# Optimization experiments

Measured on AMD Instinct MI355X. Metric: run time of the kernel, lower is better.

The kernel has to match this reference:

```python
import jax, jax.numpy as jnp
import numpy as np

PI = 3.141592657  # constant used verbatim in the original module


def _shift(a, dy, dx):
    # out[i, j] = a[i + dy, j + dx], zero-padded at the border (matches conv2d padding=1)
    h, w = a.shape
    p = jnp.pad(a, 1)
    return jax.lax.dynamic_slice(p, (1 + dy, 1 + dx), (h, w))


def setup_inputs() -> dict:
    key = jax.random.key(0)
    h, w = 2048, 4096
    # realistic metric depth in [1, 80] meters
    depth = jax.random.uniform(key, (h, w), dtype=jnp.float32, minval=1.0, maxval=80.0)
    fx = fy = 1000.0
    cx, cy = w / 2.0, h / 2.0
    cam_param = jnp.array([[fx, 0.0, cx], [0.0, fy, cy], [0.0, 0.0, 1.0]], dtype=jnp.float32)
    return {"depth": depth, "cam_param": cam_param, "sign_filter": 1}


def _nim_forward(depth, cam_param, sign_filter):
    h, w = depth.shape
    fx = cam_param[0, 0]
    fy = cam_param[1, 1]
    cx = cam_param[0, 2]
    cy = cam_param[1, 2]

    v = jnp.arange(h, dtype=jnp.float32)[:, None]
    u = jnp.arange(w, dtype=jnp.float32)[None, :]

    Z = depth
    Y = Z * (v - cy) / fx  # original uses camParam[0,0] for Y as well
    X = Z * (u - cx) / fx
    neg = Y <= 0
    Z = jnp.where(neg, 0.0, Z)
    Y = jnp.where(neg, 0.0, Y)
    Z = jnp.where(jnp.isnan(Z), 0.0, Z)

    D = 1.0 / Z  # disparity-like map; inf where Z == 0, as in torch

    # Gx = [[0,0,0],[-1,0,1],[0,0,0]], Gy = [[0,-1,0],[0,0,0],[0,1,0]] (cross-correlation)
    Gu = _shift(D, 0, 1) - _shift(D, 0, -1)
    Gv = _shift(D, 1, 0) - _shift(D, -1, 0)
    nx_t = Gu * fx
    ny_t = Gv * fy

    phi = jnp.arctan(ny_t / nx_t) + PI
    a = jnp.cos(phi)
    b = jnp.sin(phi)

    # the 4 diff kernels compute X[i,j] - X[i+dy, j+dx] for these neighbor offsets
    dirs = ((-1, 0), (0, -1), (0, 1), (1, 0))

    def diffs(A):
        return jnp.stack([A - _shift(A, dy, dx) for dy, dx in dirs])  # (4, h, w)

    X_d, Y_d, Z_d = diffs(X), diffs(Y), diffs(Z)

    nz_i = -(nx_t[None] * X_d + ny_t[None] * Y_d) / Z_d  # (4, h, w)
    norm = jnp.sqrt(nx_t[None] ** 2 + ny_t[None] ** 2 + nz_i ** 2)
    nxv = nx_t[None] / norm
    nyv = ny_t[None] / norm
    nzv = nz_i / norm
    nxv = jnp.where(jnp.isnan(nxv), 0.0, nxv)
    nyv = jnp.where(jnp.isnan(nyv), 0.0, nyv)
    nzv = jnp.where(jnp.isnan(nzv), 0.0, nzv)

    if sign_filter:
        n_pos = jnp.sum(nzv > 0, axis=0, keepdims=True)
        n_neg = jnp.sum(nzv < 0, axis=0, keepdims=True)
        pos_mask = (n_pos >= n_neg) & (nzv > 0)
        neg_mask = (n_pos < n_neg) & (nzv < 0)
        fm = (pos_mask | neg_mask).astype(jnp.float32)
        nxv = nxv * fm
        nyv = nyv * fm
        nzv = nzv * fm

    theta = jnp.arctan((jnp.sum(nxv, 0) * a + jnp.sum(nyv, 0) * b) / jnp.sum(nzv, 0))
    nx = jnp.sin(theta) * a
    ny = jnp.sin(theta) * b
    nz = jnp.cos(theta)
    bad = jnp.isnan(nz)
    nx = jnp.where(bad, 0.0, nx)
    ny = jnp.where(bad, 0.0, ny)
    nz = jnp.where(bad, -1.0, nz)

    sign_map = jnp.where(ny > 0, -1.0, 1.0)
    return jnp.stack([nx * sign_map, ny * sign_map, nz * sign_map])  # (3, h, w)


def reference(depth, cam_param, sign_filter):
    return _nim_forward(depth, cam_param, sign_filter)
```

## Files before the change

### kernel.cpp

```cpp
#include <hip/hip_runtime.h>
#include <math.h>

#define HH 2048
#define WW 4096

__device__ __forceinline__ float rcp_f(float x){ return __builtin_amdgcn_rcpf(x); }
__device__ __forceinline__ float rsq_f(float x){ return __builtin_amdgcn_rsqf(x); }

typedef float vf2 __attribute__((ext_vector_type(2)));

__device__ __forceinline__ void st_nt2(float* p, float a, float b){
    vf2 v = {a, b};
    __builtin_nontemporal_store(v, (vf2*)p);
}

__global__ __launch_bounds__(256, 6)
void nim_kernel(const float* __restrict__ depth,
                const float* __restrict__ cam,
                const int*   __restrict__ signf,
                float* __restrict__ out)
{
    const int j0 = (blockIdx.x * 256 + threadIdx.x) * 2;
    const int i  = blockIdx.y;
    const size_t HW  = (size_t)HH * WW;
    const size_t idx = (size_t)i * WW + j0;

    const float cy = cam[5];

    if ((float)i <= cy + 1.0f){
        st_nt2(out + idx,         0.f, 0.f);
        st_nt2(out + HW + idx,    0.f, 0.f);
        st_nt2(out + 2*HW + idx, -1.f,-1.f);
        return;
    }

    const float fx = cam[0], cx = cam[2], fy = cam[4];
    const float inv_fx = rcp_f(fx);
    const int   sf = signf[0];

    const float rf_u = ((float)(i - 1) - cy) * inv_fx;
    const float rf_c = ((float)i       - cy) * inv_fx;
    const float rf_d = ((float)(i + 1) - cy) * inv_fx;

    const float* rowc = depth + (size_t)i * WW + j0;
    const float* rowu = depth + (size_t)(i - 1) * WW + j0;

    float dc[4], du[2], dd[2];
    {
        const vf2 a = *(const vf2*)rowc;
        dc[1] = a.x; dc[2] = a.y;
        const vf2 ua = *(const vf2*)rowu;
        du[0] = ua.x; du[1] = ua.y;
    }
    const bool lv = (j0 > 0);
    const bool rv = (j0 + 2 < WW);
    dc[0] = lv ? rowc[-1] : 0.f;
    dc[3] = rv ? rowc[2]  : 0.f;

    const bool dv = (i + 1 < HH);
    if (dv){
        const vf2 da = *(const vf2*)(depth + (size_t)(i + 1) * WW + j0);
        dd[0] = da.x; dd[1] = da.y;
    } else {
        dd[0] = 0.f; dd[1] = 0.f;
    }

    float Dc[4], Du[2], Dd[2];
#pragma unroll
    for (int t = 0; t < 4; ++t) Dc[t] = rcp_f(dc[t]);
    if (!lv) Dc[0] = 0.f;
    if (!rv) Dc[3] = 0.f;
#pragma unroll
    for (int t = 0; t < 2; ++t){
        Du[t] = rcp_f(du[t]);
        Dd[t] = dv ? rcp_f(dd[t]) : 0.f;
    }

    const float jb = ((float)(j0 - 1) - cx) * inv_fx;

    float ox[2], oy[2], oz[2];
#pragma unroll
    for (int p = 0; p < 2; ++p){
        const float cfl = jb + (float)p       * inv_fx;
        const float cfc = jb + (float)(p + 1) * inv_fx;
        const float cfr = jb + (float)(p + 2) * inv_fx;
        const float CZ  = dc[p + 1];

        const float nx = (Dc[p + 2] - Dc[p]) * fx;
        const float ny = (Dd[p] - Du[p]) * fy;
        const float r2 = nx * nx + ny * ny;
        const float rr = rsq_f(r2);
        const float rs = copysignf(rr, nx);
        const float a  = -nx * rs;
        const float b  = -ny * rs;

        float hk[4], vzk[4];
        int npos = 0, nneg = 0;
#pragma unroll
        for (int k = 0; k < 4; ++k){
            float NZ, Xd, Yd;
            if (k == 0){ NZ = du[p];     const float w0 = CZ - NZ;
                         Xd = cfc * w0;  Yd = rf_c * CZ - rf_u * NZ; }
            else if (k == 1){ NZ = dc[p];     Xd = cfc * CZ - cfl * NZ;
                              Yd = rf_c * (CZ - NZ); }
            else if (k == 2){ NZ = dc[p + 2]; Xd = cfc * CZ - cfr * NZ;
                              Yd = rf_c * (CZ - NZ); }
            else            { NZ = dd[p];     const float w0 = CZ - NZ;
                              Xd = cfc * w0;  Yd = rf_c * CZ - rf_d * NZ; }
            const float w   = CZ - NZ;
            const float g   = nx * Xd + ny * Yd;
            const float arg = (r2 * w) * w + g * g;
            const float rn  = rsq_f(arg);
            float h  = fabsf(w) * rn;
            float vz = -g * copysignf(rn, w);
            const bool za = (arg == 0.f);
            if (za) h = 0.f;
            if (za || (w == 0.f)) vz = 0.f;
            hk[k] = h; vzk[k] = vz;
            npos += (vz > 0.f);
            nneg += (vz < 0.f);
        }

        const bool posm = (npos >= nneg);
        float H = 0.f, sz = 0.f;
#pragma unroll
        for (int k = 0; k < 4; ++k){
            const float vz = vzk[k];
            const bool keep = !sf || (posm ? (vz > 0.f) : (vz < 0.f));
            const float fm = keep ? 1.f : 0.f;
            H  += hk[k] * fm;
            sz += vz    * fm;
        }

        const float cs = copysignf(r2 * rr, nx);
        const float q  = (-cs * H) * rcp_f(sz);
        const float q2 = q * q;
        const float ct = rsq_f(1.f + q2);
        float st = q * ct;
        if (isinf(q2)) st = copysignf(1.f, q);

        float onx = st * a, ony = st * b, onz = ct;
        if (isnan(onz)){ onx = 0.f; ony = 0.f; onz = -1.f; }
        const float sgn = (ony > 0.f) ? -1.f : 1.f;
        ox[p] = onx * sgn; oy[p] = ony * sgn; oz[p] = onz * sgn;
    }

    st_nt2(out + idx,        ox[0], ox[1]);
    st_nt2(out + HW + idx,   oy[0], oy[1]);
    st_nt2(out + 2*HW + idx, oz[0], oz[1]);
}

extern "C" void kernel_launch(void* const* d_in, const int* in_sizes, int n_in,
                              void* d_out, int out_size, void* d_ws, size_t ws_size,
                              hipStream_t stream) {
    const float* depth = (const float*)d_in[0];
    const float* cam   = (const float*)d_in[1];
    const int*   signf = (const int*)d_in[2];
    float* out = (float*)d_out;

    dim3 block(256, 1, 1);
    dim3 grid(WW / (256 * 2), HH, 1);
    nim_kernel<<<grid, block, 0, stream>>>(depth, cam, signf, out);
}
```

Baseline: 133.2 us.

## Process four rows per thread to reuse vertical depth neighbors in registers

Each thread now computes a 4-row by 2-column strip, loading 6 center rows once and reusing them, together with their reciprocals, for the vertical neighbors of adjacent rows. This removes redundant global loads and rcp work for the up and down rows, and makes the grid 4x smaller in y. The cost is more registers per thread, so launch bounds drop to 4 blocks per SIMD, and there is less parallelism. The kernel is already near the write-bandwidth bound, so the gain is limited.

```diff
diff --git a/kernel.cpp b/kernel.cpp
--- a/kernel.cpp
+++ b/kernel.cpp
@@ -14,23 +14,26 @@
     __builtin_nontemporal_store(v, (vf2*)p);
 }
 
-__global__ __launch_bounds__(256, 6)
+__global__ __launch_bounds__(256, 4)
 void nim_kernel(const float* __restrict__ depth,
                 const float* __restrict__ cam,
                 const int*   __restrict__ signf,
                 float* __restrict__ out)
 {
     const int j0 = (blockIdx.x * 256 + threadIdx.x) * 2;
-    const int i  = blockIdx.y;
-    const size_t HW  = (size_t)HH * WW;
-    const size_t idx = (size_t)i * WW + j0;
+    const int i0 = blockIdx.y * 4;
+    const size_t HW = (size_t)HH * WW;
 
     const float cy = cam[5];
 
-    if ((float)i <= cy + 1.0f){
-        st_nt2(out + idx,         0.f, 0.f);
-        st_nt2(out + HW + idx,    0.f, 0.f);
-        st_nt2(out + 2*HW + idx, -1.f,-1.f);
+    if ((float)(i0 + 3) <= cy + 1.0f){
+#pragma unroll
+        for (int t = 0; t < 4; ++t){
+            const size_t idx = (size_t)(i0 + t) * WW + j0;
+            st_nt2(out + idx,         0.f, 0.f);
+            st_nt2(out + HW + idx,    0.f, 0.f);
+            st_nt2(out + 2*HW + idx, -1.f,-1.f);
+        }
         return;
     }
 
@@ -38,116 +41,128 @@
     const float inv_fx = rcp_f(fx);
     const int   sf = signf[0];
 
-    const float rf_u = ((float)(i - 1) - cy) * inv_fx;
-    const float rf_c = ((float)i       - cy) * inv_fx;
-    const float rf_d = ((float)(i + 1) - cy) * inv_fx;
-
-    const float* rowc = depth + (size_t)i * WW + j0;
-    const float* rowu = depth + (size_t)(i - 1) * WW + j0;
-
-    float dc[4], du[2], dd[2];
-    {
-        const vf2 a = *(const vf2*)rowc;
-        dc[1] = a.x; dc[2] = a.y;
-        const vf2 ua = *(const vf2*)rowu;
-        du[0] = ua.x; du[1] = ua.y;
-    }
     const bool lv = (j0 > 0);
     const bool rv = (j0 + 2 < WW);
-    dc[0] = lv ? rowc[-1] : 0.f;
-    dc[3] = rv ? rowc[2]  : 0.f;
 
-    const bool dv = (i + 1 < HH);
-    if (dv){
-        const vf2 da = *(const vf2*)(depth + (size_t)(i + 1) * WW + j0);
-        dd[0] = da.x; dd[1] = da.y;
-    } else {
-        dd[0] = 0.f; dd[1] = 0.f;
+    float dcen[6][2], Dcen[6][2];
+#pragma unroll
+    for (int t = 0; t < 6; ++t){
+        const int r = i0 - 1 + t;
+        if (r >= 0 && r < HH){
+            const vf2 v = *(const vf2*)(depth + (size_t)r * WW + j0);
+            dcen[t][0] = v.x;        dcen[t][1] = v.y;
+            Dcen[t][0] = rcp_f(v.x); Dcen[t][1] = rcp_f(v.y);
+        } else {
+            dcen[t][0] = 0.f; dcen[t][1] = 0.f;
+            Dcen[t][0] = 0.f; Dcen[t][1] = 0.f;
+        }
+    }
+    float dbl[4], dbr[4], Dbl[4], Dbr[4];
+#pragma unroll
+    for (int t = 0; t < 4; ++t){
+        const size_t rb = (size_t)(i0 + t) * WW;
+        dbl[t] = lv ? depth[rb + j0 - 1] : 0.f;
+        dbr[t] = rv ? depth[rb + j0 + 2] : 0.f;
+        Dbl[t] = lv ? rcp_f(dbl[t]) : 0.f;
+        Dbr[t] = rv ? rcp_f(dbr[t]) : 0.f;
     }
 
-    float Dc[4], Du[2], Dd[2];
+    float rf[6];
 #pragma unroll
-    for (int t = 0; t < 4; ++t) Dc[t] = rcp_f(dc[t]);
-    if (!lv) Dc[0] = 0.f;
-    if (!rv) Dc[3] = 0.f;
+    for (int t = 0; t < 6; ++t)
+        rf[t] = ((float)(i0 - 1 + t) - cy) * inv_fx;
+    const float cf[4] = { ((float)(j0 - 1) - cx) * inv_fx,
+                          ((float)(j0    ) - cx) * inv_fx,
+                          ((float)(j0 + 1) - cx) * inv_fx,
+                          ((float)(j0 + 2) - cx) * inv_fx };
+
 #pragma unroll
-    for (int t = 0; t < 2; ++t){
-        Du[t] = rcp_f(du[t]);
-        Dd[t] = dv ? rcp_f(dd[t]) : 0.f;
-    }
+    for (int t = 0; t < 4; ++t){
+        const size_t idx = (size_t)(i0 + t) * WW + j0;
+        if ((float)(i0 + t) <= cy + 1.0f){
+            st_nt2(out + idx,         0.f, 0.f);
+            st_nt2(out + HW + idx,    0.f, 0.f);
+            st_nt2(out + 2*HW + idx, -1.f,-1.f);
+            continue;
+        }
+        const int u = t + 1;
+        const float rf_u = rf[u - 1], rf_c = rf[u], rf_d = rf[u + 1];
 
-    const float jb = ((float)(j0 - 1) - cx) * inv_fx;
+        float ox[2], oy[2], oz[2];
+#pragma unroll
+        for (int p = 0; p < 2; ++p){
+            const float CZ  = dcen[u][p];
+            const float cfc = cf[p + 1];
+            const float ZL = (p == 0) ? dbl[t] : dcen[u][0];
+            const float ZR = (p == 0) ? dcen[u][1] : dbr[t];
+            const float DL = (p == 0) ? Dbl[t] : Dcen[u][0];
+            const float DR = (p == 0) ? Dcen[u][1] : Dbr[t];
+            const float cfL = cf[p];
+            const float cfR = cf[p + 2];
 
-    float ox[2], oy[2], oz[2];
+            const float nx = (DR - DL) * fx;
+            const float ny = (Dcen[u+1][p] - Dcen[u-1][p]) * fy;
+            const float r2 = nx * nx + ny * ny;
+            const float rr = rsq_f(r2);
+            const float rs = copysignf(rr, nx);
+            const float a  = -nx * rs;
+            const float b  = -ny * rs;
+
+            float hk[4], vzk[4];
+            int npos = 0, nneg = 0;
 #pragma unroll
-    for (int p = 0; p < 2; ++p){
-        const float cfl = jb + (float)p       * inv_fx;
-        const float cfc = jb + (float)(p + 1) * inv_fx;
-        const float cfr = jb + (float)(p + 2) * inv_fx;
-        const float CZ  = dc[p + 1];
+            for (int k = 0; k < 4; ++k){
+                float NZ, Xd, Yd;
+                if (k == 0){ NZ = dcen[u-1][p]; const float w0 = CZ - NZ;
+                             Xd = cfc * w0;     Yd = rf_c * CZ - rf_u * NZ; }
+                else if (k == 1){ NZ = ZL; Xd = cfc * CZ - cfL * NZ;
+                                  Yd = rf_c * (CZ - NZ); }
+                else if (k == 2){ NZ = ZR; Xd = cfc * CZ - cfR * NZ;
+                                  Yd = rf_c * (CZ - NZ); }
+                else            { NZ = dcen[u+1][p]; const float w0 = CZ - NZ;
+                                  Xd = cfc * w0;     Yd = rf_c * CZ - rf_d * NZ; }
+                const float w   = CZ - NZ;
+                const float g   = nx * Xd + ny * Yd;
+                const float arg = (r2 * w) * w + g * g;
+                const float rn  = rsq_f(arg);
+                float h  = fabsf(w) * rn;
+                float vz = -g * copysignf(rn, w);
+                const bool za = (arg == 0.f);
+                if (za) h = 0.f;
+                if (za || (w == 0.f)) vz = 0.f;
+                hk[k] = h; vzk[k] = vz;
+                npos += (vz > 0.f);
+                nneg += (vz < 0.f);
+            }
 
-        const float nx = (Dc[p + 2] - Dc[p]) * fx;
-        const float ny = (Dd[p] - Du[p]) * fy;
-        const float r2 = nx * nx + ny * ny;
-        const float rr = rsq_f(r2);
-        const float rs = copysignf(rr, nx);
-        const float a  = -nx * rs;
-        const float b  = -ny * rs;
+            const bool posm = (npos >= nneg);
+            float H = 0.f, sz = 0.f;
+#pragma unroll
+            for (int k = 0; k < 4; ++k){
+                const float vz = vzk[k];
+                const bool keep = !sf || (posm ? (vz > 0.f) : (vz < 0.f));
+                const float fm = keep ? 1.f : 0.f;
+                H  += hk[k] * fm;
+                sz += vz    * fm;
+            }
 
-        float hk[4], vzk[4];
-        int npos = 0, nneg = 0;
-#pragma unroll
-        for (int k = 0; k < 4; ++k){
-            float NZ, Xd, Yd;
-            if (k == 0){ NZ = du[p];     const float w0 = CZ - NZ;
-                         Xd = cfc * w0;  Yd = rf_c * CZ - rf_u * NZ; }
-            else if (k == 1){ NZ = dc[p];     Xd = cfc * CZ - cfl * NZ;
-                              Yd = rf_c * (CZ - NZ); }
-            else if (k == 2){ NZ = dc[p + 2]; Xd = cfc * CZ - cfr * NZ;
-                              Yd = rf_c * (CZ - NZ); }
-            else            { NZ = dd[p];     const float w0 = CZ - NZ;
-                              Xd = cfc * w0;  Yd = rf_c * CZ - rf_d * NZ; }
-            const float w   = CZ - NZ;
-            const float g   = nx * Xd + ny * Yd;
-            const float arg = (r2 * w) * w + g * g;
-            const float rn  = rsq_f(arg);
-            float h  = fabsf(w) * rn;
-            float vz = -g * copysignf(rn, w);
-            const bool za = (arg == 0.f);
-            if (za) h = 0.f;
-            if (za || (w == 0.f)) vz = 0.f;
-            hk[k] = h; vzk[k] = vz;
-            npos += (vz > 0.f);
-            nneg += (vz < 0.f);
+            const float cs = copysignf(r2 * rr, nx);
+            const float q  = (-cs * H) * rcp_f(sz);
+            const float q2 = q * q;
+            const float ct = rsq_f(1.f + q2);
+            float st = q * ct;
+            if (isinf(q2)) st = copysignf(1.f, q);
+
+            float onx = st * a, ony = st * b, onz = ct;
+            if (isnan(onz)){ onx = 0.f; ony = 0.f; onz = -1.f; }
+            const float sgn = (ony > 0.f) ? -1.f : 1.f;
+            ox[p] = onx * sgn; oy[p] = ony * sgn; oz[p] = onz * sgn;
         }
 
-        const bool posm = (npos >= nneg);
-        float H = 0.f, sz = 0.f;
-#pragma unroll
-        for (int k = 0; k < 4; ++k){
-            const float vz = vzk[k];
-            const bool keep = !sf || (posm ? (vz > 0.f) : (vz < 0.f));
-            const float fm = keep ? 1.f : 0.f;
-            H  += hk[k] * fm;
-            sz += vz    * fm;
-        }
-
-        const float cs = copysignf(r2 * rr, nx);
-        const float q  = (-cs * H) * rcp_f(sz);
-        const float q2 = q * q;
-        const float ct = rsq_f(1.f + q2);
-        float st = q * ct;
-        if (isinf(q2)) st = copysignf(1.f, q);
-
-        float onx = st * a, ony = st * b, onz = ct;
-        if (isnan(onz)){ onx = 0.f; ony = 0.f; onz = -1.f; }
-        const float sgn = (ony > 0.f) ? -1.f : 1.f;
-        ox[p] = onx * sgn; oy[p] = ony * sgn; oz[p] = onz * sgn;
+        st_nt2(out + idx,        ox[0], ox[1]);
+        st_nt2(out + HW + idx,   oy[0], oy[1]);
+        st_nt2(out + 2*HW + idx, oz[0], oz[1]);
     }
-
-    st_nt2(out + idx,        ox[0], ox[1]);
-    st_nt2(out + HW + idx,   oy[0], oy[1]);
-    st_nt2(out + 2*HW + idx, oz[0], oz[1]);
 }
 
 extern "C" void kernel_launch(void* const* d_in, const int* in_sizes, int n_in,
@@ -159,6 +174,6 @@
     float* out = (float*)d_out;
 
     dim3 block(256, 1, 1);
-    dim3 grid(WW / (256 * 2), HH, 1);
+    dim3 grid(WW / (256 * 2), HH / 4, 1);
     nim_kernel<<<grid, block, 0, stream>>>(depth, cam, signf, out);
 }
```

Result: slower. 138.2 us (+3.7%).
